# Optimization experiments

Measured on AMD Instinct MI355X. Metric: run time of the kernel, lower is better.

Reference implementation:

```python
import jax, jax.numpy as jnp
import numpy as np

B, NV, JN = 1024, 8, 21
V = NV * JN            # 168 tokens = num_view * joint_num
F_DIM, NH, DQ, DV = 512, 4, 128, 128
HID = 512
EPS = 1e-6
NEG = float(-2**32 + 1)


def _layer_norm(x, g, b):
    mu = jnp.mean(x, axis=-1, keepdims=True)
    var = jnp.mean(jnp.square(x - mu), axis=-1, keepdims=True)
    return (x - mu) * jax.lax.rsqrt(var + EPS) * g + b


def setup_inputs() -> dict:
    key = jax.random.key(0)
    ks = jax.random.split(key, 12)
    s = 0.02
    return {
        "x": jax.random.normal(ks[0], (B, V, F_DIM), dtype=jnp.float32),
        "valid": jax.random.randint(ks[1], (B, NV), 0, 2),
        "wq": jax.random.normal(ks[2], (NH * DQ, F_DIM), dtype=jnp.float32) * s,
        "bq": jnp.zeros((NH * DQ,), dtype=jnp.float32),
        "wk": jax.random.normal(ks[3], (NH * DQ, F_DIM), dtype=jnp.float32) * s,
        "bk": jnp.zeros((NH * DQ,), dtype=jnp.float32),
        "wv": jax.random.normal(ks[4], (NH * DV, F_DIM), dtype=jnp.float32) * s,
        "bv": jnp.zeros((NH * DV,), dtype=jnp.float32),
        "fc_w": jax.random.normal(ks[5], (F_DIM, NH * DV), dtype=jnp.float32) * s,
        "fc_b": jnp.zeros((F_DIM,), dtype=jnp.float32),
        "ln1_g": jnp.ones((F_DIM,), dtype=jnp.float32),
        "ln1_b": jnp.zeros((F_DIM,), dtype=jnp.float32),
        "ln2_g": jnp.ones((F_DIM,), dtype=jnp.float32),
        "ln2_b": jnp.zeros((F_DIM,), dtype=jnp.float32),
        "fc1_w": jax.random.normal(ks[6], (HID, F_DIM), dtype=jnp.float32) * s,
        "fc1_b": jnp.zeros((HID,), dtype=jnp.float32),
        "fc2_w": jax.random.normal(ks[7], (F_DIM, HID), dtype=jnp.float32) * s,
        "fc2_b": jnp.zeros((F_DIM,), dtype=jnp.float32),
    }


def reference(x, valid, wq, bq, wk, bk, wv, bv, fc_w, fc_b,
              ln1_g, ln1_b, ln2_g, ln2_b, fc1_w, fc1_b, fc2_w, fc2_b):
    bs = x.shape[0]
    h = _layer_norm(x, ln1_g, ln1_b)                          # [B,V,f]
    q = (h @ wq.T + bq).reshape(bs, V, NH, DQ)                # [B,V,H,dq]
    k = (h @ wk.T + bk).reshape(bs, V, NH, DQ)
    v = (h @ wv.T + bv).reshape(bs, V, NH, DV)
    attn = jnp.einsum('bqhd,bkhd->bhqk', q, k) / jnp.sqrt(jnp.float32(DQ))
    # valid mask: per-view validity expanded to per-token, pairwise additive
    w = jnp.where(valid == 0, NEG, 0.0).astype(x.dtype)       # [B,NV]
    w = jnp.repeat(w, JN, axis=1)                             # [B,V], view-major
    m = w[:, :, None] + w[:, None, :]                         # [B,V,V]
    attn = attn + m[:, None, :, :]
    attn = jax.nn.softmax(attn, axis=-1)
    out = jnp.einsum('bhqk,bkhd->bqhd', attn, v).reshape(bs, V, NH * DV)
    out = out @ fc_w.T + fc_b
    x = x + out
    # MLP residual block
    h2 = _layer_norm(x, ln2_g, ln2_b)
    h2 = jax.nn.relu(h2 @ fc1_w.T + fc1_b) @ fc2_w.T + fc2_b
    return x + h2
```

## Files before the change

kernel.cpp:

```cpp
#include <hip/hip_runtime.h>
#include <stdint.h>

#define BATCH 1024
#define NVIEW 8
#define JN_   21
#define VTOK  168
#define FDIM  512
#define NHEAD 4
#define DHEAD 128
#define MROWS (BATCH*VTOK)
#define SCALE2 0.127517434f

typedef __attribute__((ext_vector_type(8))) short s8v;
typedef __attribute__((ext_vector_type(4))) short s4v;
typedef __attribute__((ext_vector_type(4))) float f4v;

static __device__ __forceinline__ short f2bf(float f){
  unsigned u = __builtin_bit_cast(unsigned, f);
  unsigned r = (u + 0x7FFFu + ((u >> 16) & 1u)) >> 16;
  return (short)(unsigned short)r;
}
static __device__ __forceinline__ float bf2f(short s){
  unsigned u = ((unsigned)(unsigned short)s) << 16;
  return __builtin_bit_cast(float, u);
}

#define GL16(gp, lp) __builtin_amdgcn_global_load_lds( \
    (__attribute__((address_space(1))) void*)(gp), \
    (__attribute__((address_space(3))) void*)(lp), 16, 0, 0)

__global__ __launch_bounds__(256) void convert_w(
    const float* __restrict__ wq, const float* __restrict__ wk,
    const float* __restrict__ wv, const float* __restrict__ fcw,
    const float* __restrict__ fc1, const float* __restrict__ fc2,
    short* __restrict__ dst){
  int id = blockIdx.x * 256 + threadIdx.x;
  int e = id * 4;
  int seg = e >> 18;
  int off = e & 262143;
  const float* s = seg==0?wq: seg==1?wk: seg==2?wv: seg==3?fcw: seg==4?fc1: fc2;
  float4 u = *(const float4*)(s + off);
  s4v o; o[0]=f2bf(u.x); o[1]=f2bf(u.y); o[2]=f2bf(u.z); o[3]=f2bf(u.w);
  *(s4v*)(dst + e) = o;
}

__global__ __launch_bounds__(256) void ln1_kernel(
    const float* __restrict__ x, const float* __restrict__ g,
    const float* __restrict__ bb, short* __restrict__ h){
  int row  = blockIdx.x * 4 + (threadIdx.x >> 6);
  int lane = threadIdx.x & 63;
  size_t base = (size_t)row * 512 + lane * 8;
  float4 u0 = *(const float4*)(x + base);
  float4 u1 = *(const float4*)(x + base + 4);
  float s = u0.x+u0.y+u0.z+u0.w + u1.x+u1.y+u1.z+u1.w;
  float q = u0.x*u0.x+u0.y*u0.y+u0.z*u0.z+u0.w*u0.w
          + u1.x*u1.x+u1.y*u1.y+u1.z*u1.z+u1.w*u1.w;
  #pragma unroll
  for (int o = 1; o < 64; o <<= 1){ s += __shfl_xor(s,o); q += __shfl_xor(q,o); }
  float mu = s * (1.f/512.f);
  float rstd = rsqrtf(q*(1.f/512.f) - mu*mu + 1e-6f);
  float4 g0 = *(const float4*)(g + lane*8),  g1 = *(const float4*)(g + lane*8 + 4);
  float4 b0 = *(const float4*)(bb + lane*8), b1 = *(const float4*)(bb + lane*8 + 4);
  s8v o_;
  o_[0]=f2bf((u0.x-mu)*rstd*g0.x+b0.x); o_[1]=f2bf((u0.y-mu)*rstd*g0.y+b0.y);
  o_[2]=f2bf((u0.z-mu)*rstd*g0.z+b0.z); o_[3]=f2bf((u0.w-mu)*rstd*g0.w+b0.w);
  o_[4]=f2bf((u1.x-mu)*rstd*g1.x+b1.x); o_[5]=f2bf((u1.y-mu)*rstd*g1.y+b1.y);
  o_[6]=f2bf((u1.z-mu)*rstd*g1.z+b1.z); o_[7]=f2bf((u1.w-mu)*rstd*g1.w+b1.w);
  *(s8v*)(h + base) = o_;
}

__global__ __launch_bounds__(256) void resid_ln(
    const float* __restrict__ x, const short* __restrict__ y,
    const float* __restrict__ g, const float* __restrict__ bb,
    short* __restrict__ x2b, short* __restrict__ g2){
  int row  = blockIdx.x * 4 + (threadIdx.x >> 6);
  int lane = threadIdx.x & 63;
  size_t base = (size_t)row * 512 + lane * 8;
  float4 u0 = *(const float4*)(x + base);
  float4 u1 = *(const float4*)(x + base + 4);
  s8v yv = *(const s8v*)(y + base);
  float v[8];
  v[0]=u0.x+bf2f(yv[0]); v[1]=u0.y+bf2f(yv[1]); v[2]=u0.z+bf2f(yv[2]); v[3]=u0.w+bf2f(yv[3]);
  v[4]=u1.x+bf2f(yv[4]); v[5]=u1.y+bf2f(yv[5]); v[6]=u1.z+bf2f(yv[6]); v[7]=u1.w+bf2f(yv[7]);
  s8v xv;
  #pragma unroll
  for (int i = 0; i < 8; i++) xv[i] = f2bf(v[i]);
  *(s8v*)(x2b + base) = xv;
  float s = 0.f, q = 0.f;
  #pragma unroll
  for (int i = 0; i < 8; i++){ s += v[i]; q += v[i]*v[i]; }
  #pragma unroll
  for (int o = 1; o < 64; o <<= 1){ s += __shfl_xor(s,o); q += __shfl_xor(q,o); }
  float mu = s * (1.f/512.f);
  float rstd = rsqrtf(q*(1.f/512.f) - mu*mu + 1e-6f);
  float4 g0 = *(const float4*)(g + lane*8),  g1 = *(const float4*)(g + lane*8 + 4);
  float4 b0 = *(const float4*)(bb + lane*8), b1 = *(const float4*)(bb + lane*8 + 4);
  s8v o_;
  o_[0]=f2bf((v[0]-mu)*rstd*g0.x+b0.x); o_[1]=f2bf((v[1]-mu)*rstd*g0.y+b0.y);
  o_[2]=f2bf((v[2]-mu)*rstd*g0.z+b0.z); o_[3]=f2bf((v[3]-mu)*rstd*g0.w+b0.w);
  o_[4]=f2bf((v[4]-mu)*rstd*g1.x+b1.x); o_[5]=f2bf((v[5]-mu)*rstd*g1.y+b1.y);
  o_[6]=f2bf((v[6]-mu)*rstd*g1.z+b1.z); o_[7]=f2bf((v[7]-mu)*rstd*g1.w+b1.w);
  *(s8v*)(g2 + base) = o_;
}

template<int MODE>
__global__ __launch_bounds__(512, 1) void gemm_bt(
    const short* __restrict__ A, const short* __restrict__ Bm,
    const float* __restrict__ bias0, const float* __restrict__ bias1,
    const short* __restrict__ aux, short* __restrict__ out0,
    short* __restrict__ out1, float* __restrict__ outf){
  __shared__ short lds[81920];
  short* const AL = lds;
  short* const BL = lds + 49152;
  const int tid = threadIdx.x, lane = tid & 63;
  const int wid = tid >> 6, wr = wid >> 2, wc = wid & 3;
  const int lg = lane >> 4, l15 = lane & 15, l7 = lane & 7;
  const int nwg  = gridDim.x * gridDim.y;
  const int flat = blockIdx.y * gridDim.x + blockIdx.x;
  const int swz  = (flat & 7) * (nwg >> 3) + (flat >> 3);
  size_t mt, nt;
  if (MODE == 1){ mt = swz & 1; nt = (size_t)(swz >> 1); }
  else {
    constexpr int GX = (MODE == 0) ? 4 : 2;
    nt = swz % GX; mt = swz / GX;
  }
  const size_t m0 = mt * 256, n0 = nt * 256;
  const short* Ab = A + m0 * 512;
  const short* Bb = Bm + n0 * 512;

#define STAGEA(slot, tile, half) do {                                   \
    const short* s_ = Ab + (size_t)(half)*65536 + (tile)*64;            \
    short* d_ = AL + (slot)*8192;                                       \
    _Pragma("unroll")                                                   \
    for (int r_ = 0; r_ < 2; r_++){                                     \
      int c_ = r_*512 + tid;                                            \
      int row_ = c_ >> 3, chk_ = (c_ & 7) ^ (row_ & 7);                 \
      GL16(s_ + (size_t)row_*512 + chk_*8, d_ + c_*8);                  \
    } } while(0)
#define STAGEB(slot, tile, half) do {                                   \
    const short* s_ = Bb + (size_t)(half)*65536 + (tile)*64;            \
    short* d_ = BL + (slot)*8192;                                       \
    _Pragma("unroll")                                                   \
    for (int r_ = 0; r_ < 2; r_++){                                     \
      int c_ = r_*512 + tid;                                            \
      int row_ = c_ >> 3, chk_ = (c_ & 7) ^ (row_ & 7);                 \
      GL16(s_ + (size_t)row_*512 + chk_*8, d_ + c_*8);                  \
    } } while(0)
#define PWAIT() do {                                                    \
    __builtin_amdgcn_s_barrier();                                       \
    asm volatile("s_waitcnt lgkmcnt(0)" ::: "memory");                  \
    __builtin_amdgcn_sched_barrier(0); } while(0)

  STAGEA(0, 0, 0); STAGEA(1, 0, 1);
  STAGEB(0, 0, 0); STAGEB(1, 0, 1);
  STAGEA(2, 1, 0); STAGEA(3, 1, 1);
  asm volatile("s_waitcnt vmcnt(4)" ::: "memory");
  __builtin_amdgcn_s_barrier();

  f4v acc[8][4];
  #pragma unroll
  for (int m=0;m<8;m++)
    #pragma unroll
    for (int n=0;n<4;n++) acc[m][n] = f4v{0.f,0.f,0.f,0.f};

  s8v b0[4], b1[4], a[4];
  #pragma unroll
  for (int t = 0; t < 8; ++t){
    const short* Awp = AL + ((2*t)%6 + wr)*8192 + l15*64;
    const short* Bwp = BL + ((2*t)%4 + (wc>>1))*8192 + ((wc&1)*64 + l15)*64;
    const int c0 = (lg ^ l7) * 8;
    const int c1 = ((4 + lg) ^ l7) * 8;
    #pragma unroll
    for (int n=0;n<4;n++) b0[n] = *(const s8v*)(Bwp + n*1024 + c0);
    #pragma unroll
    for (int m=0;m<4;m++) a[m]  = *(const s8v*)(Awp + m*1024 + c0);
    if (t < 7) STAGEB((2*t+2)%4, t+1, 0);
    PWAIT();
    __builtin_amdgcn_s_setprio(1);
    #pragma unroll
    for (int m=0;m<4;m++)
      #pragma unroll
      for (int n=0;n<4;n++)
        acc[m][n] = __builtin_amdgcn_mfma_f32_16x16x32_bf16(a[m], b0[n], acc[m][n], 0,0,0);
    __builtin_amdgcn_s_setprio(0);
    __builtin_amdgcn_s_barrier();
    #pragma unroll
    for (int m=0;m<4;m++) a[m] = *(const s8v*)(Awp + (64+m*16)*64 + c0);
    if (t < 7) STAGEB((2*t+2)%4 + 1, t+1, 1);
    PWAIT();
    __builtin_amdgcn_s_setprio(1);
    #pragma unroll
    for (int m=0;m<4;m++)
      #pragma unroll
      for (int n=0;n<4;n++)
        acc[4+m][n] = __builtin_amdgcn_mfma_f32_16x16x32_bf16(a[m], b0[n], acc[4+m][n], 0,0,0);
    __builtin_amdgcn_s_setprio(0);
    __builtin_amdgcn_s_barrier();
    #pragma unroll
    for (int n=0;n<4;n++) b1[n] = *(const s8v*)(Bwp + n*1024 + c1);
    #pragma unroll
    for (int m=0;m<4;m++) a[m]  = *(const s8v*)(Awp + m*1024 + c1);
    if (t < 6) STAGEA((2*t+4)%6, t+2, 0);
    PWAIT();
    __builtin_amdgcn_s_setprio(1);
    #pragma unroll
    for (int m=0;m<4;m++)
      #pragma unroll
      for (int n=0;n<4;n++)
        acc[m][n] = __builtin_amdgcn_mfma_f32_16x16x32_bf16(a[m], b1[n], acc[m][n], 0,0,0);
    __builtin_amdgcn_s_setprio(0);
    __builtin_amdgcn_s_barrier();
    #pragma unroll
    for (int m=0;m<4;m++) a[m] = *(const s8v*)(Awp + (64+m*16)*64 + c1);
    if (t < 6) STAGEA((2*t+4)%6 + 1, t+2, 1);
    PWAIT();
    __builtin_amdgcn_s_setprio(1);
    #pragma unroll
    for (int m=0;m<4;m++)
      #pragma unroll
      for (int n=0;n<4;n++)
        acc[4+m][n] = __builtin_amdgcn_mfma_f32_16x16x32_bf16(a[m], b1[n], acc[4+m][n], 0,0,0);
    __builtin_amdgcn_s_setprio(0);
    if (t < 6)       asm volatile("s_waitcnt vmcnt(4)" ::: "memory");
    else if (t == 6) asm volatile("s_waitcnt vmcnt(0)" ::: "memory");
    __builtin_amdgcn_s_barrier();
  }
#undef STAGEA
#undef STAGEB
#undef PWAIT

  #pragma unroll
  for (int m=0;m<8;m++)
  #pragma unroll
  for (int n=0;n<4;n++)
  #pragma unroll
  for (int r=0;r<4;r++){
    int rowL = wr*128 + m*16 + lg*4 + r;
    int colL = wc*64 + n*16 + l15;
    size_t gm = m0 + rowL, gn = n0 + colL;
    float val = acc[m][n][r];
    if (MODE == 0){
      int nn = (int)gn;
      val += (nn < 512) ? bias0[nn] : bias1[nn - 512];
      int head = (nn >> 7) & 3, d = nn & 127;
      size_t b = gm / 168, tok = gm - b * 168;
      size_t idx = ((b*4 + head)*168 + tok)*128 + d;
      ((nn < 512) ? out0 : out1)[idx] = f2bf(val);
    } else if (MODE == 1){
      val += bias0[gm];
      int hh = ((int)gm >> 7) & 3, d = (int)gm & 127;
      size_t b = gn / 168, tok = gn - b * 168;
      out0[((b*4 + hh)*128 + d)*168 + tok] = f2bf(val);
    } else if (MODE == 2 || MODE == 3){
      val += bias0[gn];
      if (MODE == 3) val = fmaxf(val, 0.f);
      out0[gm*512 + gn] = f2bf(val);
    } else {
      val += bias0[gn] + bf2f(aux[gm*512 + gn]);
      outf[gm*512 + gn] = val;
    }
  }
}

__global__ __launch_bounds__(256, 2) void attn_kernel(
    const short* __restrict__ qg_, const short* __restrict__ kg_,
    const short* __restrict__ vtg_, const int* __restrict__ valid,
    short* __restrict__ outp){
  __shared__ short Ps[192*200];

  int tid = threadIdx.x, lane = tid & 63, wid = tid >> 6;
  int lg = lane >> 4, l15 = lane & 15;
  int bh = blockIdx.x, b = bh >> 2, hh = bh & 3;
  const short* qg  = qg_  + (size_t)bh * (168*128);
  const short* kg  = kg_  + (size_t)bh * (168*128);
  const short* vtg = vtg_ + (size_t)bh * (128*168);

  int bits = 0;
  #pragma unroll
  for (int v = 0; v < 8; v++) bits |= (valid[b*8 + v] != 0) << v;
  if (bits == 0) bits = 255;
  float wk2[11];
  #pragma unroll
  for (int n = 0; n < 11; n++){
    int kt = n*16 + l15;
    int view = (kt * 781) >> 14;
    wk2[n] = ((bits >> view) & 1) ? 0.0f : -1.0e9f;
  }

  int row0 = wid * 48;
  f4v zf = {0.f,0.f,0.f,0.f};

  s8v qf[3][4];
  #pragma unroll
  for (int m=0;m<3;m++)
    #pragma unroll
    for (int kf=0;kf<4;kf++)
      qf[m][kf] = *(const s8v*)(qg + (size_t)(row0 + m*16 + l15)*128 + kf*32 + lg*8);

  f4v accS[3][11];
  #pragma unroll
  for (int m=0;m<3;m++)
    #pragma unroll
    for (int n=0;n<11;n++) accS[m][n] = zf;
  s8v kb[2][4];
  #pragma unroll
  for (int kf=0;kf<4;kf++)
    kb[0][kf] = *(const s8v*)(kg + (size_t)l15*128 + kf*32 + lg*8);
  #pragma unroll
  for (int n=0;n<11;n++){
    if (n < 10){
      #pragma unroll
      for (int kf=0;kf<4;kf++)
        kb[(n+1)&1][kf] = *(const s8v*)(kg + (size_t)((n+1)*16 + l15)*128 + kf*32 + lg*8);
    }
    __builtin_amdgcn_s_setprio(1);
    #pragma unroll
    for (int kf=0;kf<4;kf++)
      #pragma unroll
      for (int m=0;m<3;m++)
        accS[m][n] = __builtin_amdgcn_mfma_f32_16x16x32_bf16(qf[m][kf], kb[n&1][kf], accS[m][n], 0,0,0);
    __builtin_amdgcn_s_setprio(0);
  }

  float inv_[3][4];
  #pragma unroll
  for (int m=0;m<3;m++){
    #pragma unroll
    for (int r=0;r<4;r++){
      int qtok = row0 + m*16 + lg*4 + r;
      float sum = 0.f;
      #pragma unroll
      for (int n=0;n<11;n++){
        float p = exp2f(fmaf(accS[m][n][r], SCALE2, wk2[n]));
        sum += p;
        Ps[qtok*200 + n*16 + l15] = f2bf(p);
      }
      sum += __shfl_xor(sum,1); sum += __shfl_xor(sum,2);
      sum += __shfl_xor(sum,4); sum += __shfl_xor(sum,8);
      inv_[m][r] = 1.0f / sum;
    }
  }
  {
    s8v z8 = {0,0,0,0,0,0,0,0};
    for (int i = lane; i < 96; i += 64){
      int rr = row0 + (i >> 1);
      *(s8v*)&Ps[rr*200 + 176 + (i&1)*8] = z8;
    }
  }

  s8v ap[3][6];
  #pragma unroll
  for (int m=0;m<3;m++)
    #pragma unroll
    for (int kf=0;kf<6;kf++)
      ap[m][kf] = *(const s8v*)&Ps[(row0 + m*16 + l15)*200 + kf*32 + lg*8];

  f4v accO[3][8];
  #pragma unroll
  for (int m=0;m<3;m++)
    #pragma unroll
    for (int n=0;n<8;n++) accO[m][n] = zf;
  s8v vb[2][6];
  #pragma unroll
  for (int kf=0;kf<6;kf++)
    vb[0][kf] = *(const s8v*)(vtg + (size_t)l15*168 + kf*32 + lg*8);
  #pragma unroll
  for (int n=0;n<8;n++){
    if (n < 7){
      #pragma unroll
      for (int kf=0;kf<6;kf++)
        vb[(n+1)&1][kf] = *(const s8v*)(vtg + (size_t)((n+1)*16 + l15)*168 + kf*32 + lg*8);
    }
    __builtin_amdgcn_s_setprio(1);
    #pragma unroll
    for (int kf=0;kf<6;kf++)
      #pragma unroll
      for (int m=0;m<3;m++)
        accO[m][n] = __builtin_amdgcn_mfma_f32_16x16x32_bf16(ap[m][kf], vb[n&1][kf], accO[m][n], 0,0,0);
    __builtin_amdgcn_s_setprio(0);
  }

  #pragma unroll
  for (int m=0;m<3;m++){
    #pragma unroll
    for (int r=0;r<4;r++){
      int qtok = row0 + m*16 + lg*4 + r;
      if (qtok < 168){
        float iv = inv_[m][r];
        size_t base = ((size_t)b*168 + qtok)*512 + hh*128;
        #pragma unroll
        for (int n=0;n<8;n++)
          outp[base + n*16 + l15] = f2bf(accO[m][n][r] * iv);
      }
    }
  }
}

extern "C" void kernel_launch(void* const* d_in, const int* in_sizes, int n_in,
                              void* d_out, int out_size, void* d_ws, size_t ws_size,
                              hipStream_t stream) {
  const float* x     = (const float*)d_in[0];
  const int*   valid = (const int*)  d_in[1];
  const float* wq    = (const float*)d_in[2];
  const float* bq    = (const float*)d_in[3];
  const float* wk    = (const float*)d_in[4];
  const float* bk    = (const float*)d_in[5];
  const float* wv    = (const float*)d_in[6];
  const float* bv    = (const float*)d_in[7];
  const float* fcw   = (const float*)d_in[8];
  const float* fcb   = (const float*)d_in[9];
  const float* ln1g  = (const float*)d_in[10];
  const float* ln1b  = (const float*)d_in[11];
  const float* ln2g  = (const float*)d_in[12];
  const float* ln2b  = (const float*)d_in[13];
  const float* fc1w  = (const float*)d_in[14];
  const float* fc1b  = (const float*)d_in[15];
  const float* fc2w  = (const float*)d_in[16];
  const float* fc2b  = (const float*)d_in[17];

  char* ws = (char*)d_ws;
  short* h       = (short*)(ws + 0LL);
  short* q_ws    = (short*)(ws + 176160768LL);
  short* k_ws    = (short*)(ws + 352321536LL);
  short* vt_ws   = (short*)(ws + 528482304LL);
  short* wb      = (short*)(ws + 704643072LL);
  short* attn_o  = h;
  short* y       = q_ws;
  short* g2      = h;
  short* a1      = k_ws;
  short* x2b     = vt_ws;
  float* outp    = (float*)d_out;

  convert_w<<<1536, 256, 0, stream>>>(wq, wk, wv, fcw, fc1w, fc2w, wb);
  ln1_kernel<<<MROWS/4, 256, 0, stream>>>(x, ln1g, ln1b, h);
  gemm_bt<0><<<dim3(4, MROWS/256), 512, 0, stream>>>(h, wb, bq, bk, nullptr, q_ws, k_ws, nullptr);
  gemm_bt<1><<<dim3(2, MROWS/256), 512, 0, stream>>>(wb + 524288, h, bv, nullptr, nullptr, vt_ws, nullptr, nullptr);
  attn_kernel<<<BATCH*NHEAD, 256, 0, stream>>>(q_ws, k_ws, vt_ws, valid, attn_o);
  gemm_bt<2><<<dim3(2, MROWS/256), 512, 0, stream>>>(attn_o, wb + 786432, fcb, nullptr, nullptr, y, nullptr, nullptr);
  resid_ln<<<MROWS/4, 256, 0, stream>>>(x, y, ln2g, ln2b, x2b, g2);
  gemm_bt<3><<<dim3(2, MROWS/256), 512, 0, stream>>>(g2, wb + 1048576, fc1b, nullptr, nullptr, a1, nullptr, nullptr);
  gemm_bt<4><<<dim3(2, MROWS/256), 512, 0, stream>>>(a1, wb + 1310720, fc2b, nullptr, x2b, nullptr, nullptr, outp);
}
```

Measured before the change: 1.268 ms.

## Stage K tiles in LDS for attention and deepen V prefetch

In the attention kernel, the whole per-head K tile is now loaded once into LDS (swizzled) with async global-to-LDS copies. This shared LDS buffer is aliased with the P scratch, so the four waves no longer each fetch K from global memory separately. V prefetch goes from double to triple buffering. In the GEMM main loop the explicit lgkmcnt wait and sched_barrier after each barrier are removed, and the second B fragment register set is dropped to reduce register pressure. The risks are a longer serialized K prologue and reliance on compiler-inserted LDS waits.

Result: no change. 1.248 ms (-1.6%).

```diff
diff --git a/kernel.cpp b/kernel.cpp
--- a/kernel.cpp
+++ b/kernel.cpp
@@ -146,10 +146,6 @@
       int row_ = c_ >> 3, chk_ = (c_ & 7) ^ (row_ & 7);                 \
       GL16(s_ + (size_t)row_*512 + chk_*8, d_ + c_*8);                  \
     } } while(0)
-#define PWAIT() do {                                                    \
-    __builtin_amdgcn_s_barrier();                                       \
-    asm volatile("s_waitcnt lgkmcnt(0)" ::: "memory");                  \
-    __builtin_amdgcn_sched_barrier(0); } while(0)
 
   STAGEA(0, 0, 0); STAGEA(1, 0, 1);
   STAGEB(0, 0, 0); STAGEB(1, 0, 1);
@@ -163,7 +159,7 @@
     #pragma unroll
     for (int n=0;n<4;n++) acc[m][n] = f4v{0.f,0.f,0.f,0.f};
 
-  s8v b0[4], b1[4], a[4];
+  s8v b0[4], a[4];
   #pragma unroll
   for (int t = 0; t < 8; ++t){
     const short* Awp = AL + ((2*t)%6 + wr)*8192 + l15*64;
@@ -175,7 +171,7 @@
     #pragma unroll
     for (int m=0;m<4;m++) a[m]  = *(const s8v*)(Awp + m*1024 + c0);
     if (t < 7) STAGEB((2*t+2)%4, t+1, 0);
-    PWAIT();
+    __builtin_amdgcn_s_barrier();
     __builtin_amdgcn_s_setprio(1);
     #pragma unroll
     for (int m=0;m<4;m++)
@@ -187,7 +183,7 @@
     #pragma unroll
     for (int m=0;m<4;m++) a[m] = *(const s8v*)(Awp + (64+m*16)*64 + c0);
     if (t < 7) STAGEB((2*t+2)%4 + 1, t+1, 1);
-    PWAIT();
+    __builtin_amdgcn_s_barrier();
     __builtin_amdgcn_s_setprio(1);
     #pragma unroll
     for (int m=0;m<4;m++)
@@ -197,29 +193,29 @@
     __builtin_amdgcn_s_setprio(0);
     __builtin_amdgcn_s_barrier();
     #pragma unroll
-    for (int n=0;n<4;n++) b1[n] = *(const s8v*)(Bwp + n*1024 + c1);
+    for (int n=0;n<4;n++) b0[n] = *(const s8v*)(Bwp + n*1024 + c1);
     #pragma unroll
     for (int m=0;m<4;m++) a[m]  = *(const s8v*)(Awp + m*1024 + c1);
     if (t < 6) STAGEA((2*t+4)%6, t+2, 0);
-    PWAIT();
+    __builtin_amdgcn_s_barrier();
     __builtin_amdgcn_s_setprio(1);
     #pragma unroll
     for (int m=0;m<4;m++)
       #pragma unroll
       for (int n=0;n<4;n++)
-        acc[m][n] = __builtin_amdgcn_mfma_f32_16x16x32_bf16(a[m], b1[n], acc[m][n], 0,0,0);
+        acc[m][n] = __builtin_amdgcn_mfma_f32_16x16x32_bf16(a[m], b0[n], acc[m][n], 0,0,0);
     __builtin_amdgcn_s_setprio(0);
     __builtin_amdgcn_s_barrier();
     #pragma unroll
     for (int m=0;m<4;m++) a[m] = *(const s8v*)(Awp + (64+m*16)*64 + c1);
     if (t < 6) STAGEA((2*t+4)%6 + 1, t+2, 1);
-    PWAIT();
+    __builtin_amdgcn_s_barrier();
     __builtin_amdgcn_s_setprio(1);
     #pragma unroll
     for (int m=0;m<4;m++)
       #pragma unroll
       for (int n=0;n<4;n++)
-        acc[4+m][n] = __builtin_amdgcn_mfma_f32_16x16x32_bf16(a[m], b1[n], acc[4+m][n], 0,0,0);
+        acc[4+m][n] = __builtin_amdgcn_mfma_f32_16x16x32_bf16(a[m], b0[n], acc[4+m][n], 0,0,0);
     __builtin_amdgcn_s_setprio(0);
     if (t < 6)       asm volatile("s_waitcnt vmcnt(4)" ::: "memory");
     else if (t == 6) asm volatile("s_waitcnt vmcnt(0)" ::: "memory");
@@ -227,7 +223,6 @@
   }
 #undef STAGEA
 #undef STAGEB
-#undef PWAIT
 
   #pragma unroll
   for (int m=0;m<8;m++)
@@ -266,7 +261,9 @@
     const short* __restrict__ qg_, const short* __restrict__ kg_,
     const short* __restrict__ vtg_, const int* __restrict__ valid,
     short* __restrict__ outp){
-  __shared__ short Ps[192*200];
+  __shared__ short ldsb[38400];
+  short* const Kl = ldsb;
+  short* const Ps = ldsb;
 
   int tid = threadIdx.x, lane = tid & 63, wid = tid >> 6;
   int lg = lane >> 4, l15 = lane & 15;
@@ -275,6 +272,14 @@
   const short* kg  = kg_  + (size_t)bh * (168*128);
   const short* vtg = vtg_ + (size_t)bh * (128*168);
 
+  #pragma unroll
+  for (int r = 0; r < 11; r++){
+    int c = r*256 + tid;
+    int row = c >> 4;
+    int g = (c & 15) ^ ((row & 1) << 2);
+    GL16(kg + (size_t)row*128 + g*8, Kl + c*8);
+  }
+
   int bits = 0;
   #pragma unroll
   for (int v = 0; v < 8; v++) bits |= (valid[b*8 + v] != 0) << v;
@@ -297,30 +302,29 @@
     for (int kf=0;kf<4;kf++)
       qf[m][kf] = *(const s8v*)(qg + (size_t)(row0 + m*16 + l15)*128 + kf*32 + lg*8);
 
+  asm volatile("s_waitcnt vmcnt(0)" ::: "memory");
+  __builtin_amdgcn_s_barrier();
+
   f4v accS[3][11];
   #pragma unroll
   for (int m=0;m<3;m++)
     #pragma unroll
     for (int n=0;n<11;n++) accS[m][n] = zf;
-  s8v kb[2][4];
-  #pragma unroll
-  for (int kf=0;kf<4;kf++)
-    kb[0][kf] = *(const s8v*)(kg + (size_t)l15*128 + kf*32 + lg*8);
   #pragma unroll
   for (int n=0;n<11;n++){
-    if (n < 10){
-      #pragma unroll
-      for (int kf=0;kf<4;kf++)
-        kb[(n+1)&1][kf] = *(const s8v*)(kg + (size_t)((n+1)*16 + l15)*128 + kf*32 + lg*8);
-    }
-    __builtin_amdgcn_s_setprio(1);
+    s8v kb[4];
     #pragma unroll
     for (int kf=0;kf<4;kf++)
+      kb[kf] = *(const s8v*)&Kl[(size_t)(n*16 + l15)*128 + (((kf*4 + lg) ^ ((l15 & 1) << 2)) << 3)];
+    __builtin_amdgcn_s_setprio(1);
+    #pragma unroll
+    for (int kf=0;kf<4;kf++)
       #pragma unroll
       for (int m=0;m<3;m++)
-        accS[m][n] = __builtin_amdgcn_mfma_f32_16x16x32_bf16(qf[m][kf], kb[n&1][kf], accS[m][n], 0,0,0);
-    __builtin_amdgcn_s_setprio(0);
-  }
+        accS[m][n] = __builtin_amdgcn_mfma_f32_16x16x32_bf16(qf[m][kf], kb[kf], accS[m][n], 0,0,0);
+    __builtin_amdgcn_s_setprio(0);
+  }
+  __builtin_amdgcn_s_barrier();
 
   float inv_[3][4];
   #pragma unroll
@@ -360,23 +364,25 @@
   for (int m=0;m<3;m++)
     #pragma unroll
     for (int n=0;n<8;n++) accO[m][n] = zf;
-  s8v vb[2][6];
-  #pragma unroll
-  for (int kf=0;kf<6;kf++)
-    vb[0][kf] = *(const s8v*)(vtg + (size_t)l15*168 + kf*32 + lg*8);
+  s8v vb[3][6];
+  #pragma unroll
+  for (int p=0;p<2;p++)
+    #pragma unroll
+    for (int kf=0;kf<6;kf++)
+      vb[p][kf] = *(const s8v*)(vtg + (size_t)(p*16 + l15)*168 + kf*32 + lg*8);
   #pragma unroll
   for (int n=0;n<8;n++){
-    if (n < 7){
+    if (n < 6){
       #pragma unroll
       for (int kf=0;kf<6;kf++)
-        vb[(n+1)&1][kf] = *(const s8v*)(vtg + (size_t)((n+1)*16 + l15)*168 + kf*32 + lg*8);
+        vb[(n+2)%3][kf] = *(const s8v*)(vtg + (size_t)((n+2)*16 + l15)*168 + kf*32 + lg*8);
     }
     __builtin_amdgcn_s_setprio(1);
     #pragma unroll
     for (int kf=0;kf<6;kf++)
       #pragma unroll
       for (int m=0;m<3;m++)
-        accO[m][n] = __builtin_amdgcn_mfma_f32_16x16x32_bf16(ap[m][kf], vb[n&1][kf], accO[m][n], 0,0,0);
+        accO[m][n] = __builtin_amdgcn_mfma_f32_16x16x32_bf16(ap[m][kf], vb[n%3][kf], accO[m][n], 0,0,0);
     __builtin_amdgcn_s_setprio(0);
   }
 
```
